# Kernel tuning notes

Hardware: AMD Instinct MI355X
Metric: run time of the kernel (lower is better)

## Reference

```python
import jax, jax.numpy as jnp
import numpy as np

N = 500000      # active voxels
C_IN = 16       # input voxel feature dim
# encoder channels per stage: 32, 64, 128


def setup_inputs() -> dict:
    key = jax.random.key(0)
    ks = jax.random.split(key, 16)

    def w(k, i, o):
        return jax.random.normal(k, (i, o), dtype=jnp.float32) * (1.0 / np.sqrt(i))

    d = {}
    d['feat'] = jax.random.normal(ks[0], (N, C_IN), dtype=jnp.float32)
    d['coords'] = jax.random.randint(ks[1], (N, 4), 0, 1024, dtype=jnp.int32)
    d['W_in'] = w(ks[2], C_IN, 32)
    d['W_enc1'] = w(ks[3], 32, 32)
    d['W_enc2'] = w(ks[4], 32, 64)
    d['W_enc3'] = w(ks[5], 64, 128)
    d['W_lat1'] = w(ks[6], 32, 32)
    d['W_lat2'] = w(ks[7], 64, 64)
    d['W_lat3'] = w(ks[8], 128, 128)
    d['W_merge1'] = w(ks[9], 64, 32)    # merge: 2*C_i -> C_i
    d['W_merge2'] = w(ks[10], 128, 64)
    d['W_merge3'] = w(ks[11], 256, 128)
    d['W_up1'] = w(ks[12], 32, 32)      # upsample: C_i -> C_{i-1}
    d['W_up2'] = w(ks[13], 64, 32)
    d['W_up3'] = w(ks[14], 128, 64)
    return d


def _forward(feat, W_in, W_enc1, W_enc2, W_enc3, W_lat1, W_lat2, W_lat3,
             W_merge1, W_merge2, W_merge3, W_up1, W_up2, W_up3):
    relu = jax.nn.relu
    # conv_input + encoder (1x1 submanifold sparse convs == per-voxel matmul)
    x = relu(feat @ W_in)
    e1 = relu(x @ W_enc1)
    e2 = relu(e1 @ W_enc2)
    e3 = relu(e2 @ W_enc3)
    enc = [e1, e2, e3]
    lats = [W_lat1, W_lat2, W_lat3]
    mrgs = [W_merge1, W_merge2, W_merge3]
    ups = [W_up1, W_up2, W_up3]
    x = e3
    for i in (2, 1, 0):  # decoder stages stage_num..1
        lat = relu(enc[i] @ lats[i])                    # lateral_layer
        # cat0(x_bottom) + cat1(lat): identity-placement 1x1 convs == concat
        cat = jnp.concatenate([x, lat], axis=-1)        # [N, 2*C_i]
        merge = relu(cat @ mrgs[i])                     # merge_layer 2C->C
        red = cat.reshape(cat.shape[0], -1, 2).sum(-1)  # reduce_channel: fixed pairwise-sum conv
        x = relu((merge + red) @ ups[i])                # residual add + upsample_layer
    return x  # ret['voxel_feats']


def reference(feat, coords, W_in, W_enc1, W_enc2, W_enc3, W_lat1, W_lat2, W_lat3,
              W_merge1, W_merge2, W_merge3, W_up1, W_up2, W_up3):
    # coords define sparse structure; for 1x1 subm convs the math only touches features
    return _forward(feat, W_in, W_enc1, W_enc2, W_enc3, W_lat1, W_lat2, W_lat3,
                    W_merge1, W_merge2, W_merge3, W_up1, W_up2, W_up3)
```

## Files before the change

kernel.cpp:

```cpp
#include <hip/hip_runtime.h>

typedef unsigned short u16;
typedef unsigned int u32;
typedef _Float16 h16;
typedef __attribute__((ext_vector_type(2))) _Float16 half2v;
typedef __attribute__((ext_vector_type(8))) _Float16 half8;
typedef __attribute__((ext_vector_type(8))) unsigned short ushort8;
typedef __attribute__((ext_vector_type(4))) float f32x4;

#define NPAIRS 15625
#define STRIPH 12032

#define AE1 0
#define SE1 40
#define AE2 1280
#define SE2 72
#define ACT 3584
#define SCT 264
#define AMR 3712
#define SMR 264

#define MFMA16(A,B,C) __builtin_amdgcn_mfma_f32_16x16x32_f16(A,B,C,0,0,0)

#define LBAR() asm volatile("s_waitcnt lgkmcnt(0)\n\ts_barrier" ::: "memory")

#define F_L0   0
#define F_L1   2
#define F_L2   4
#define F_L3   8
#define F_L4   24
#define F_L5   56
#define F_L6   120
#define F_L7   136
#define F_L8   144
#define F_L9   160
#define F_L10  164
#define F_L11  166
#define F_L12  170
#define NFRAG  172

__device__ __forceinline__ u16 hb(h16 h) { union { h16 h; u16 u; } v; v.h = h; return v.u; }

__global__ __launch_bounds__(256) void pack_w(
    const float* w0, const float* w1, const float* w2, const float* w3, const float* w4,
    const float* w5, const float* w6, const float* w7, const float* w8, const float* w9,
    const float* w10, const float* w11, const float* w12, u16* __restrict__ packed)
{
  const float* ws[13] = {w0,w1,w2,w3,w4,w5,w6,w7,w8,w9,w10,w11,w12};
  const int Ka[13]  = {16,32,32,64,128,256,128,64,128,64,32,64,32};
  const int KT[13]  = {1,1,1,2,4,8,4,2,4,2,1,2,1};
  const int CO[13]  = {32,32,64,128,128,128,64,64,64,32,32,32,32};
  const int FO[13]  = {F_L0,F_L1,F_L2,F_L3,F_L4,F_L5,F_L6,F_L7,F_L8,F_L9,F_L10,F_L11,F_L12};
  int g = blockIdx.x * 256 + threadIdx.x;
  int f = g >> 6, lane = g & 63;
  if (f >= NFRAG) return;
  int layer = 0;
#pragma unroll
  for (int i = 1; i < 13; ++i) if (f >= FO[i]) layer = i;
  int fl = f - FO[layer];
  int kt = fl % KT[layer];
  int ct = fl / KT[layer];
  int cout = CO[layer];
  int quad = lane >> 4;
  int col  = ct * 16 + (lane & 15);
  u16 thi[8], tlo[8];
#pragma unroll
  for (int j = 0; j < 8; ++j) {
    int k = kt * 32 + quad * 8 + j;
    float w = (k < Ka[layer]) ? ws[layer][k * cout + col] : 0.f;
    h16 h = (h16)w;
    h16 l = (h16)(w - (float)h);
    thi[j] = hb(h); tlo[j] = hb(l);
  }
  u16* dst = packed + ((size_t)f * 64 + lane) * 16;
  *(ushort8*)dst       = *(const ushort8*)thi;
  *(ushort8*)(dst + 8) = *(const ushort8*)tlo;
}


__device__ __forceinline__ void splitw(h16* dst, int idx, int dlo, float v) {
  h16 h = (h16)v;
  dst[idx]       = h;
  dst[idx + dlo] = (h16)(v - (float)h);
}

__device__ __forceinline__ float red2p(const h16* cat, int cs, int rr, int cc) {
  half2v hp = *reinterpret_cast<const half2v*>(cat + rr * cs + 2 * cc);
  half2v lp = *reinterpret_cast<const half2v*>(cat + (rr + 16) * cs + 2 * cc);
  return (float)hp.x + (float)hp.y + (float)lp.x + (float)lp.y;
}

template<int KT, int EPI, int BAR>
__device__ __forceinline__ void layerW(
    const h16* __restrict__ asrc, int as,
    const h16* __restrict__ wp, int foff, int ct, int lane,
    half8 pbh, half8 pbl,
    h16* dst, int ds, int colb, const h16* cat, int cs,
    float* __restrict__ gout, int row0)
{
  const int l15 = lane & 15, quad = lane >> 4;
  const int abase = l15 * as + quad * 8;
  const int alo = 16 * as;
  f32x4 a0 = {0.f,0.f,0.f,0.f}, a1 = {0.f,0.f,0.f,0.f};
#pragma unroll
  for (int kt = 0; kt < KT; ++kt) {
    half8 bhv, blv;
    if (kt == 0) { bhv = pbh; blv = pbl; }
    else {
      const h16* fp = wp + (((size_t)(foff + ct * KT + kt)) * 64 + lane) * 16;
      bhv = *(const half8*)fp;
      blv = *(const half8*)(fp + 8);
    }
    const h16* p0 = asrc + abase + kt * 32;
    const h16* p1 = p0 + STRIPH;
    half8 ah0 = *(const half8*)p0;
    half8 al0 = *(const half8*)(p0 + alo);
    half8 ah1 = *(const half8*)p1;
    half8 al1 = *(const half8*)(p1 + alo);
    a0 = MFMA16(al0, bhv, a0); a0 = MFMA16(ah0, blv, a0); a0 = MFMA16(ah0, bhv, a0);
    a1 = MFMA16(al1, bhv, a1); a1 = MFMA16(ah1, blv, a1); a1 = MFMA16(ah1, bhv, a1);
  }
  const int cc = ct * 16 + l15;
  float v0r[4], v1r[4];
#pragma unroll
  for (int r = 0; r < 4; ++r) {
    const int rr = quad * 4 + r;
    float v0 = a0[r] > 0.f ? a0[r] : 0.f;
    float v1 = a1[r] > 0.f ? a1[r] : 0.f;
    if (EPI == 1) {
      v0 += red2p(cat, cs, rr, cc);
      v1 += red2p(cat + STRIPH, cs, rr, cc);
    }
    v0r[r] = v0; v1r[r] = v1;
  }
  if (BAR) LBAR();
  if (EPI <= 1) {
    const int dlo = 16 * ds;
#pragma unroll
    for (int r = 0; r < 4; ++r) {
      const int rr = quad * 4 + r;
      const int idx = rr * ds + colb + cc;
      splitw(dst,          idx, dlo, v0r[r]);
      splitw(dst + STRIPH, idx, dlo, v1r[r]);
    }
  } else {
#pragma unroll
    for (int r = 0; r < 4; ++r) {
      const int rr = quad * 4 + r;
      gout[(size_t)(row0 + rr) * 32 + cc]      = v0r[r];
      gout[(size_t)(row0 + 16 + rr) * 32 + cc] = v1r[r];
    }
  }
}

#define PFB(FOFF, CIDX, KT_)                                                        \
  do { const h16* _fp = wp + (((size_t)((FOFF) + (CIDX) * (KT_))) * 64 + lane) * 16; \
       pbh = *(const half8*)_fp; pbl = *(const half8*)(_fp + 8); } while (0)

__global__ __launch_bounds__(512, 6) void backbone(
    const float* __restrict__ feat, const h16* __restrict__ wp, float* __restrict__ out)
{
  __shared__ h16 lds[2 * STRIPH];
  const int lane = threadIdx.x & 63;
  const int wv   = threadIdx.x >> 6;
  const int l15 = lane & 15, quad = lane >> 4;
  const int row0 = blockIdx.x * 32;

  h16* E1 = lds + AE1;
  h16* E2 = lds + AE2;
  h16* CT = lds + ACT;
  h16* MR = lds + AMR;

  half8 pbh, pbl;

  if (wv < 2) {
    PFB(F_L0, wv, 1);
    h16 th0[8] = {0,0,0,0,0,0,0,0}, tl0[8] = {0,0,0,0,0,0,0,0};
    h16 th1[8] = {0,0,0,0,0,0,0,0}, tl1[8] = {0,0,0,0,0,0,0,0};
    if (quad < 2) {
      const float* s0 = feat + (size_t)(row0 + l15) * 16 + quad * 8;
      const float* s1 = feat + (size_t)(row0 + 16 + l15) * 16 + quad * 8;
      f32x4 u0a = *(const f32x4*)s0, u0b = *(const f32x4*)(s0 + 4);
      f32x4 u1a = *(const f32x4*)s1, u1b = *(const f32x4*)(s1 + 4);
#pragma unroll
      for (int j = 0; j < 4; ++j) {
        h16 h;
        h = (h16)u0a[j]; th0[j]   = h; tl0[j]   = (h16)(u0a[j] - (float)h);
        h = (h16)u0b[j]; th0[4+j] = h; tl0[4+j] = (h16)(u0b[j] - (float)h);
        h = (h16)u1a[j]; th1[j]   = h; tl1[j]   = (h16)(u1a[j] - (float)h);
        h = (h16)u1b[j]; th1[4+j] = h; tl1[4+j] = (h16)(u1b[j] - (float)h);
      }
    }
    half8 ah0 = *(const half8*)th0, al0 = *(const half8*)tl0;
    half8 ah1 = *(const half8*)th1, al1 = *(const half8*)tl1;
    f32x4 a0 = {0.f,0.f,0.f,0.f}, a1 = {0.f,0.f,0.f,0.f};
    a0 = MFMA16(al0, pbh, a0); a0 = MFMA16(ah0, pbl, a0); a0 = MFMA16(ah0, pbh, a0);
    a1 = MFMA16(al1, pbh, a1); a1 = MFMA16(ah1, pbl, a1); a1 = MFMA16(ah1, pbh, a1);
    const int dlo = 16 * SCT;
#pragma unroll
    for (int r = 0; r < 4; ++r) {
      const int rr = quad * 4 + r;
      const int idx = rr * SCT + wv * 16 + l15;
      splitw(CT,          idx, dlo, a0[r] > 0.f ? a0[r] : 0.f);
      splitw(CT + STRIPH, idx, dlo, a1[r] > 0.f ? a1[r] : 0.f);
    }
    PFB(F_L1, wv, 1);
  }
  LBAR();

  if (wv < 2) {
    layerW<1,0,0>(CT,SCT, wp, F_L1, wv, lane, pbh,pbl, E1,SE1,0, nullptr,0, nullptr,0);
  }
  if (wv < 4) PFB(F_L2, wv, 1);
  LBAR();

  if (wv < 4) {
    layerW<1,0,0>(E1,SE1, wp, F_L2, wv, lane, pbh,pbl, E2,SE2,0, nullptr,0, nullptr,0);
  }
  PFB(F_L3, wv, 2);
  LBAR();

  layerW<2,0,0>(E2,SE2, wp, F_L3, wv, lane, pbh,pbl, CT,SCT,0, nullptr,0, nullptr,0);
  PFB(F_L4, wv, 4);
  LBAR();

  layerW<4,0,0>(CT,SCT, wp, F_L4, wv, lane, pbh,pbl, CT,SCT,128, nullptr,0, nullptr,0);
  PFB(F_L5, wv, 8);
  LBAR();

  layerW<8,1,1>(CT,SCT, wp, F_L5, wv, lane, pbh,pbl, MR,SMR,0, CT,SCT, nullptr,0);
  if (wv < 4) PFB(F_L6, wv, 4); else PFB(F_L7, wv - 4, 2);
  LBAR();

  if (wv < 4) {
    layerW<4,0,0>(MR,SMR, wp, F_L6, wv, lane, pbh,pbl, CT,SCT,0,  nullptr,0, nullptr,0);
  } else {
    layerW<2,0,0>(E2,SE2, wp, F_L7, wv - 4, lane, pbh,pbl, CT,SCT,64, nullptr,0, nullptr,0);
  }
  if (wv < 4) PFB(F_L8, wv, 4);
  LBAR();

  if (wv < 4) {
    layerW<4,1,0>(CT,SCT, wp, F_L8, wv, lane, pbh,pbl, MR,SMR,0, CT,SCT, nullptr,0);
  }
  if (wv < 2) PFB(F_L9, wv, 2);
  else if (wv < 4) PFB(F_L10, wv - 2, 1);
  LBAR();

  if (wv < 2) {
    layerW<2,0,0>(MR,SMR, wp, F_L9, wv, lane, pbh,pbl, CT,SCT,0,  nullptr,0, nullptr,0);
  } else if (wv < 4) {
    layerW<1,0,0>(E1,SE1, wp, F_L10, wv - 2, lane, pbh,pbl, CT,SCT,32, nullptr,0, nullptr,0);
  }
  if (wv < 2) PFB(F_L11, wv, 2);
  LBAR();

  if (wv < 2) {
    layerW<2,1,0>(CT,SCT, wp, F_L11, wv, lane, pbh,pbl, MR,SMR,0, CT,SCT, nullptr,0);
    PFB(F_L12, wv, 1);
  }
  LBAR();

  if (wv < 2) {
    layerW<1,2,0>(MR,SMR, wp, F_L12, wv, lane, pbh,pbl, nullptr,0,0, nullptr,0, out, row0);
  }
}

extern "C" void kernel_launch(void* const* d_in, const int* in_sizes, int n_in,
                              void* d_out, int out_size, void* d_ws, size_t ws_size,
                              hipStream_t stream) {
  (void)in_sizes; (void)n_in; (void)out_size; (void)ws_size;
  u16* packed = (u16*)d_ws;

  hipLaunchKernelGGL(pack_w, dim3(43), dim3(256), 0, stream,
      (const float*)d_in[2],  (const float*)d_in[3],  (const float*)d_in[4],
      (const float*)d_in[5],  (const float*)d_in[8],  (const float*)d_in[11],
      (const float*)d_in[14], (const float*)d_in[7],  (const float*)d_in[10],
      (const float*)d_in[13], (const float*)d_in[6],  (const float*)d_in[9],
      (const float*)d_in[12], packed);

  hipLaunchKernelGGL(backbone, dim3(NPAIRS), dim3(512), 0, stream,
                     (const float*)d_in[0], (const h16*)packed, (float*)d_out);
}
```

Before: 432.3 us.

## Remap warp work so each wave computes two column tiles for one row strip

Each wave used to compute one 16-column output tile for both 16-row strips, sharing one B fragment across two A fragments. Now each wave handles one row strip and two adjacent column tiles, so one A fragment (hi/lo) is reused across two weight fragments. This doubles the weight loads per wave and halves the LDS activation reads. It also spreads the first layer over four waves instead of two. The change shifts the bottleneck from LDS reads toward global/L2 weight fetches and adds more prefetch registers.

Result: slower. 459.8 us (+6.4%).

```diff
diff --git a/kernel.cpp b/kernel.cpp
--- a/kernel.cpp
+++ b/kernel.cpp
@@ -91,45 +91,43 @@
 }
 
 template<int KT, int EPI, int BAR>
-__device__ __forceinline__ void layerW(
+__device__ __forceinline__ void layer1(
     const h16* __restrict__ asrc, int as,
-    const h16* __restrict__ wp, int foff, int ct, int lane,
-    half8 pbh, half8 pbl,
+    const h16* __restrict__ wp, int foff, int ct0, int lane,
+    half8 pbh, half8 pbl, half8 pbh2, half8 pbl2,
     h16* dst, int ds, int colb, const h16* cat, int cs,
-    float* __restrict__ gout, int row0)
+    float* __restrict__ gout, int grow0)
 {
   const int l15 = lane & 15, quad = lane >> 4;
   const int abase = l15 * as + quad * 8;
   const int alo = 16 * as;
-  f32x4 a0 = {0.f,0.f,0.f,0.f}, a1 = {0.f,0.f,0.f,0.f};
+  f32x4 acc0 = {0.f,0.f,0.f,0.f}, acc1 = {0.f,0.f,0.f,0.f};
 #pragma unroll
   for (int kt = 0; kt < KT; ++kt) {
-    half8 bhv, blv;
-    if (kt == 0) { bhv = pbh; blv = pbl; }
+    const h16* p0 = asrc + abase + kt * 32;
+    half8 ah = *(const half8*)p0;
+    half8 al = *(const half8*)(p0 + alo);
+    half8 b0h, b0l, b1h, b1l;
+    if (kt == 0) { b0h = pbh; b0l = pbl; b1h = pbh2; b1l = pbl2; }
     else {
-      const h16* fp = wp + (((size_t)(foff + ct * KT + kt)) * 64 + lane) * 16;
-      bhv = *(const half8*)fp;
-      blv = *(const half8*)(fp + 8);
-    }
-    const h16* p0 = asrc + abase + kt * 32;
-    const h16* p1 = p0 + STRIPH;
-    half8 ah0 = *(const half8*)p0;
-    half8 al0 = *(const half8*)(p0 + alo);
-    half8 ah1 = *(const half8*)p1;
-    half8 al1 = *(const half8*)(p1 + alo);
-    a0 = MFMA16(al0, bhv, a0); a0 = MFMA16(ah0, blv, a0); a0 = MFMA16(ah0, bhv, a0);
-    a1 = MFMA16(al1, bhv, a1); a1 = MFMA16(ah1, blv, a1); a1 = MFMA16(ah1, bhv, a1);
-  }
-  const int cc = ct * 16 + l15;
+      const h16* f0 = wp + (((size_t)(foff + ct0 * KT + kt)) * 64 + lane) * 16;
+      const h16* f1 = wp + (((size_t)(foff + (ct0 + 1) * KT + kt)) * 64 + lane) * 16;
+      b0h = *(const half8*)f0; b0l = *(const half8*)(f0 + 8);
+      b1h = *(const half8*)f1; b1l = *(const half8*)(f1 + 8);
+    }
+    acc0 = MFMA16(al, b0h, acc0); acc0 = MFMA16(ah, b0l, acc0); acc0 = MFMA16(ah, b0h, acc0);
+    acc1 = MFMA16(al, b1h, acc1); acc1 = MFMA16(ah, b1l, acc1); acc1 = MFMA16(ah, b1h, acc1);
+  }
+  const int cc0 = ct0 * 16 + l15, cc1 = cc0 + 16;
   float v0r[4], v1r[4];
 #pragma unroll
   for (int r = 0; r < 4; ++r) {
     const int rr = quad * 4 + r;
-    float v0 = a0[r] > 0.f ? a0[r] : 0.f;
-    float v1 = a1[r] > 0.f ? a1[r] : 0.f;
+    float v0 = acc0[r] > 0.f ? acc0[r] : 0.f;
+    float v1 = acc1[r] > 0.f ? acc1[r] : 0.f;
     if (EPI == 1) {
-      v0 += red2p(cat, cs, rr, cc);
-      v1 += red2p(cat + STRIPH, cs, rr, cc);
+      v0 += red2p(cat, cs, rr, cc0);
+      v1 += red2p(cat, cs, rr, cc1);
     }
     v0r[r] = v0; v1r[r] = v1;
   }
@@ -139,16 +137,15 @@
 #pragma unroll
     for (int r = 0; r < 4; ++r) {
       const int rr = quad * 4 + r;
-      const int idx = rr * ds + colb + cc;
-      splitw(dst,          idx, dlo, v0r[r]);
-      splitw(dst + STRIPH, idx, dlo, v1r[r]);
+      splitw(dst, rr * ds + colb + cc0, dlo, v0r[r]);
+      splitw(dst, rr * ds + colb + cc1, dlo, v1r[r]);
     }
   } else {
 #pragma unroll
     for (int r = 0; r < 4; ++r) {
       const int rr = quad * 4 + r;
-      gout[(size_t)(row0 + rr) * 32 + cc]      = v0r[r];
-      gout[(size_t)(row0 + 16 + rr) * 32 + cc] = v1r[r];
+      gout[(size_t)(grow0 + rr) * 32 + cc0] = v0r[r];
+      gout[(size_t)(grow0 + rr) * 32 + cc1] = v1r[r];
     }
   }
 }
@@ -156,6 +153,9 @@
 #define PFB(FOFF, CIDX, KT_)                                                        \
   do { const h16* _fp = wp + (((size_t)((FOFF) + (CIDX) * (KT_))) * 64 + lane) * 16; \
        pbh = *(const half8*)_fp; pbl = *(const half8*)(_fp + 8); } while (0)
+#define PFB2(FOFF, CIDX, KT_)                                                       \
+  do { const h16* _fp = wp + (((size_t)((FOFF) + (CIDX) * (KT_))) * 64 + lane) * 16; \
+       pbh2 = *(const half8*)_fp; pbl2 = *(const half8*)(_fp + 8); } while (0)
 
 __global__ __launch_bounds__(512, 6) void backbone(
     const float* __restrict__ feat, const h16* __restrict__ wp, float* __restrict__ out)
@@ -165,104 +165,114 @@
   const int wv   = threadIdx.x >> 6;
   const int l15 = lane & 15, quad = lane >> 4;
   const int row0 = blockIdx.x * 32;
-
-  h16* E1 = lds + AE1;
-  h16* E2 = lds + AE2;
-  h16* CT = lds + ACT;
-  h16* MR = lds + AMR;
-
-  half8 pbh, pbl;
-
-  if (wv < 2) {
-    PFB(F_L0, wv, 1);
-    h16 th0[8] = {0,0,0,0,0,0,0,0}, tl0[8] = {0,0,0,0,0,0,0,0};
-    h16 th1[8] = {0,0,0,0,0,0,0,0}, tl1[8] = {0,0,0,0,0,0,0,0};
+  const int c2 = (wv >> 1) * 2;
+  h16* Sb8 = lds + (wv & 1) * STRIPH;
+
+  half8 pbh, pbl, pbh2, pbl2;
+
+  if (wv < 4) {
+    const int st = wv >> 1, ct = wv & 1;
+    PFB(F_L0, ct, 1);
+    h16 th[8] = {0,0,0,0,0,0,0,0}, tl[8] = {0,0,0,0,0,0,0,0};
     if (quad < 2) {
-      const float* s0 = feat + (size_t)(row0 + l15) * 16 + quad * 8;
-      const float* s1 = feat + (size_t)(row0 + 16 + l15) * 16 + quad * 8;
-      f32x4 u0a = *(const f32x4*)s0, u0b = *(const f32x4*)(s0 + 4);
-      f32x4 u1a = *(const f32x4*)s1, u1b = *(const f32x4*)(s1 + 4);
+      const float* s = feat + (size_t)(row0 + st * 16 + l15) * 16 + quad * 8;
+      f32x4 ua = *(const f32x4*)s, ub = *(const f32x4*)(s + 4);
 #pragma unroll
       for (int j = 0; j < 4; ++j) {
         h16 h;
-        h = (h16)u0a[j]; th0[j]   = h; tl0[j]   = (h16)(u0a[j] - (float)h);
-        h = (h16)u0b[j]; th0[4+j] = h; tl0[4+j] = (h16)(u0b[j] - (float)h);
-        h = (h16)u1a[j]; th1[j]   = h; tl1[j]   = (h16)(u1a[j] - (float)h);
-        h = (h16)u1b[j]; th1[4+j] = h; tl1[4+j] = (h16)(u1b[j] - (float)h);
+        h = (h16)ua[j]; th[j]   = h; tl[j]   = (h16)(ua[j] - (float)h);
+        h = (h16)ub[j]; th[4+j] = h; tl[4+j] = (h16)(ub[j] - (float)h);
       }
     }
-    half8 ah0 = *(const half8*)th0, al0 = *(const half8*)tl0;
-    half8 ah1 = *(const half8*)th1, al1 = *(const half8*)tl1;
-    f32x4 a0 = {0.f,0.f,0.f,0.f}, a1 = {0.f,0.f,0.f,0.f};
-    a0 = MFMA16(al0, pbh, a0); a0 = MFMA16(ah0, pbl, a0); a0 = MFMA16(ah0, pbh, a0);
-    a1 = MFMA16(al1, pbh, a1); a1 = MFMA16(ah1, pbl, a1); a1 = MFMA16(ah1, pbh, a1);
+    half8 ah = *(const half8*)th, al = *(const half8*)tl;
+    f32x4 a = {0.f,0.f,0.f,0.f};
+    a = MFMA16(al, pbh, a); a = MFMA16(ah, pbl, a); a = MFMA16(ah, pbh, a);
+    h16* dstS = lds + st * STRIPH + ACT;
     const int dlo = 16 * SCT;
 #pragma unroll
     for (int r = 0; r < 4; ++r) {
       const int rr = quad * 4 + r;
-      const int idx = rr * SCT + wv * 16 + l15;
-      splitw(CT,          idx, dlo, a0[r] > 0.f ? a0[r] : 0.f);
-      splitw(CT + STRIPH, idx, dlo, a1[r] > 0.f ? a1[r] : 0.f);
-    }
-    PFB(F_L1, wv, 1);
-  }
-  LBAR();
-
-  if (wv < 2) {
-    layerW<1,0,0>(CT,SCT, wp, F_L1, wv, lane, pbh,pbl, E1,SE1,0, nullptr,0, nullptr,0);
-  }
-  if (wv < 4) PFB(F_L2, wv, 1);
-  LBAR();
-
-  if (wv < 4) {
-    layerW<1,0,0>(E1,SE1, wp, F_L2, wv, lane, pbh,pbl, E2,SE2,0, nullptr,0, nullptr,0);
-  }
-  PFB(F_L3, wv, 2);
-  LBAR();
-
-  layerW<2,0,0>(E2,SE2, wp, F_L3, wv, lane, pbh,pbl, CT,SCT,0, nullptr,0, nullptr,0);
-  PFB(F_L4, wv, 4);
-  LBAR();
-
-  layerW<4,0,0>(CT,SCT, wp, F_L4, wv, lane, pbh,pbl, CT,SCT,128, nullptr,0, nullptr,0);
-  PFB(F_L5, wv, 8);
-  LBAR();
-
-  layerW<8,1,1>(CT,SCT, wp, F_L5, wv, lane, pbh,pbl, MR,SMR,0, CT,SCT, nullptr,0);
-  if (wv < 4) PFB(F_L6, wv, 4); else PFB(F_L7, wv - 4, 2);
-  LBAR();
-
-  if (wv < 4) {
-    layerW<4,0,0>(MR,SMR, wp, F_L6, wv, lane, pbh,pbl, CT,SCT,0,  nullptr,0, nullptr,0);
+      splitw(dstS, rr * SCT + ct * 16 + l15, dlo, a[r] > 0.f ? a[r] : 0.f);
+    }
+  }
+  if (wv < 2) { PFB(F_L1, 0, 1); PFB2(F_L1, 1, 1); }
+  LBAR();
+
+  if (wv < 2) {
+    h16* Sb = lds + wv * STRIPH;
+    layer1<1,0,0>(Sb + ACT, SCT, wp, F_L1, 0, lane, pbh,pbl,pbh2,pbl2,
+                  Sb + AE1, SE1, 0, nullptr, 0, nullptr, 0);
+  }
+  if (wv < 4) { PFB(F_L2, c2, 1); PFB2(F_L2, c2 + 1, 1); }
+  LBAR();
+
+  if (wv < 4) {
+    layer1<1,0,0>(Sb8 + AE1, SE1, wp, F_L2, c2, lane, pbh,pbl,pbh2,pbl2,
+                  Sb8 + AE2, SE2, 0, nullptr, 0, nullptr, 0);
+  }
+  PFB(F_L3, c2, 2); PFB2(F_L3, c2 + 1, 2);
+  LBAR();
+
+  layer1<2,0,0>(Sb8 + AE2, SE2, wp, F_L3, c2, lane, pbh,pbl,pbh2,pbl2,
+                Sb8 + ACT, SCT, 0, nullptr, 0, nullptr, 0);
+  PFB(F_L4, c2, 4); PFB2(F_L4, c2 + 1, 4);
+  LBAR();
+
+  layer1<4,0,0>(Sb8 + ACT, SCT, wp, F_L4, c2, lane, pbh,pbl,pbh2,pbl2,
+                Sb8 + ACT, SCT, 128, nullptr, 0, nullptr, 0);
+  PFB(F_L5, c2, 8); PFB2(F_L5, c2 + 1, 8);
+  LBAR();
+
+  layer1<8,1,1>(Sb8 + ACT, SCT, wp, F_L5, c2, lane, pbh,pbl,pbh2,pbl2,
+                Sb8 + AMR, SMR, 0, Sb8 + ACT, SCT, nullptr, 0);
+  if (wv < 4) { PFB(F_L6, c2, 4); PFB2(F_L6, c2 + 1, 4); }
+  else        { const int w = wv - 4; PFB(F_L7, (w>>1)*2, 2); PFB2(F_L7, (w>>1)*2 + 1, 2); }
+  LBAR();
+
+  if (wv < 4) {
+    layer1<4,0,0>(Sb8 + AMR, SMR, wp, F_L6, c2, lane, pbh,pbl,pbh2,pbl2,
+                  Sb8 + ACT, SCT, 0, nullptr, 0, nullptr, 0);
   } else {
-    layerW<2,0,0>(E2,SE2, wp, F_L7, wv - 4, lane, pbh,pbl, CT,SCT,64, nullptr,0, nullptr,0);
-  }
-  if (wv < 4) PFB(F_L8, wv, 4);
-  LBAR();
-
-  if (wv < 4) {
-    layerW<4,1,0>(CT,SCT, wp, F_L8, wv, lane, pbh,pbl, MR,SMR,0, CT,SCT, nullptr,0);
-  }
-  if (wv < 2) PFB(F_L9, wv, 2);
-  else if (wv < 4) PFB(F_L10, wv - 2, 1);
-  LBAR();
-
-  if (wv < 2) {
-    layerW<2,0,0>(MR,SMR, wp, F_L9, wv, lane, pbh,pbl, CT,SCT,0,  nullptr,0, nullptr,0);
+    const int w = wv - 4;
+    h16* Sb = lds + (w & 1) * STRIPH;
+    layer1<2,0,0>(Sb + AE2, SE2, wp, F_L7, (w>>1)*2, lane, pbh,pbl,pbh2,pbl2,
+                  Sb + ACT, SCT, 64, nullptr, 0, nullptr, 0);
+  }
+  if (wv < 4) { PFB(F_L8, c2, 4); PFB2(F_L8, c2 + 1, 4); }
+  LBAR();
+
+  if (wv < 4) {
+    layer1<4,1,0>(Sb8 + ACT, SCT, wp, F_L8, c2, lane, pbh,pbl,pbh2,pbl2,
+                  Sb8 + AMR, SMR, 0, Sb8 + ACT, SCT, nullptr, 0);
+  }
+  if (wv < 2)      { PFB(F_L9, 0, 2);  PFB2(F_L9, 1, 2); }
+  else if (wv < 4) { PFB(F_L10, 0, 1); PFB2(F_L10, 1, 1); }
+  LBAR();
+
+  if (wv < 2) {
+    h16* Sb = lds + wv * STRIPH;
+    layer1<2,0,0>(Sb + AMR, SMR, wp, F_L9, 0, lane, pbh,pbl,pbh2,pbl2,
+                  Sb + ACT, SCT, 0, nullptr, 0, nullptr, 0);
   } else if (wv < 4) {
-    layerW<1,0,0>(E1,SE1, wp, F_L10, wv - 2, lane, pbh,pbl, CT,SCT,32, nullptr,0, nullptr,0);
-  }
-  if (wv < 2) PFB(F_L11, wv, 2);
-  LBAR();
-
-  if (wv < 2) {
-    layerW<2,1,0>(CT,SCT, wp, F_L11, wv, lane, pbh,pbl, MR,SMR,0, CT,SCT, nullptr,0);
-    PFB(F_L12, wv, 1);
-  }
-  LBAR();
-
-  if (wv < 2) {
-    layerW<1,2,0>(MR,SMR, wp, F_L12, wv, lane, pbh,pbl, nullptr,0,0, nullptr,0, out, row0);
+    h16* Sb = lds + (wv - 2) * STRIPH;
+    layer1<1,0,0>(Sb + AE1, SE1, wp, F_L10, 0, lane, pbh,pbl,pbh2,pbl2,
+                  Sb + ACT, SCT, 32, nullptr, 0, nullptr, 0);
+  }
+  if (wv < 2) { PFB(F_L11, 0, 2); PFB2(F_L11, 1, 2); }
+  LBAR();
+
+  if (wv < 2) {
+    h16* Sb = lds + wv * STRIPH;
+    layer1<2,1,0>(Sb + ACT, SCT, wp, F_L11, 0, lane, pbh,pbl,pbh2,pbl2,
+                  Sb + AMR, SMR, 0, Sb + ACT, SCT, nullptr, 0);
+    PFB(F_L12, 0, 1); PFB2(F_L12, 1, 1);
+  }
+  LBAR();
+
+  if (wv < 2) {
+    h16* Sb = lds + wv * STRIPH;
+    layer1<1,2,0>(Sb + AMR, SMR, wp, F_L12, 0, lane, pbh,pbl,pbh2,pbl2,
+                  nullptr, 0, 0, nullptr, 0, out, row0 + wv * 16);
   }
 }
 
```

## Split narrow layers across strips per wave and swizzle LDS columns

Applied to the files above, without the earlier changes.

Narrow layers used to run on only 2 or 4 waves, each handling both 16-row strips. They now run on twice as many waves, each handling a single strip (unitS), so more waves do useful work at those stages. The lat2/merge2 stage is fused so all 8 waves run both pieces back to back, using a second prefetched weight register pair. An XOR swizzle is also applied to the LDS column indices on both read and write, aimed at reducing bank conflicts. The cost is more register pressure from the extra prefetch and more complicated indexing that must stay consistent for correctness.

Measured after the change: 438.3 us. Within noise of the previous version (+1.4%).

```diff
diff --git a/kernel.cpp b/kernel.cpp
--- a/kernel.cpp
+++ b/kernel.cpp
@@ -84,9 +84,9 @@
   dst[idx + dlo] = (h16)(v - (float)h);
 }
 
-__device__ __forceinline__ float red2p(const h16* cat, int cs, int rr, int cc) {
-  half2v hp = *reinterpret_cast<const half2v*>(cat + rr * cs + 2 * cc);
-  half2v lp = *reinterpret_cast<const half2v*>(cat + (rr + 16) * cs + 2 * cc);
+__device__ __forceinline__ float red2s(const h16* cat, int cs, int rr, int ccr) {
+  half2v hp = *reinterpret_cast<const half2v*>(cat + rr * cs + ccr);
+  half2v lp = *reinterpret_cast<const half2v*>(cat + (rr + 16) * cs + ccr);
   return (float)hp.x + (float)hp.y + (float)lp.x + (float)lp.y;
 }
 
@@ -99,7 +99,8 @@
     float* __restrict__ gout, int row0)
 {
   const int l15 = lane & 15, quad = lane >> 4;
-  const int abase = l15 * as + quad * 8;
+  const int qsw = quad ^ ((l15 >> 3) << 1);
+  const int abase = l15 * as + qsw * 8;
   const int alo = 16 * as;
   f32x4 a0 = {0.f,0.f,0.f,0.f}, a1 = {0.f,0.f,0.f,0.f};
 #pragma unroll
@@ -120,7 +121,10 @@
     a0 = MFMA16(al0, bhv, a0); a0 = MFMA16(ah0, blv, a0); a0 = MFMA16(ah0, bhv, a0);
     a1 = MFMA16(al1, bhv, a1); a1 = MFMA16(ah1, blv, a1); a1 = MFMA16(ah1, bhv, a1);
   }
-  const int cc = ct * 16 + l15;
+  const int csw = (quad & 2) << 3;
+  const int cc  = ct * 16 + l15;
+  const int ccw = (colb + cc) ^ csw;
+  const int ccr = (2 * cc) ^ csw;
   float v0r[4], v1r[4];
 #pragma unroll
   for (int r = 0; r < 4; ++r) {
@@ -128,8 +132,8 @@
     float v0 = a0[r] > 0.f ? a0[r] : 0.f;
     float v1 = a1[r] > 0.f ? a1[r] : 0.f;
     if (EPI == 1) {
-      v0 += red2p(cat, cs, rr, cc);
-      v1 += red2p(cat + STRIPH, cs, rr, cc);
+      v0 += red2s(cat, cs, rr, ccr);
+      v1 += red2s(cat + STRIPH, cs, rr, ccr);
     }
     v0r[r] = v0; v1r[r] = v1;
   }
@@ -139,9 +143,8 @@
 #pragma unroll
     for (int r = 0; r < 4; ++r) {
       const int rr = quad * 4 + r;
-      const int idx = rr * ds + colb + cc;
-      splitw(dst,          idx, dlo, v0r[r]);
-      splitw(dst + STRIPH, idx, dlo, v1r[r]);
+      splitw(dst,          rr * ds + ccw, dlo, v0r[r]);
+      splitw(dst + STRIPH, rr * ds + ccw, dlo, v1r[r]);
     }
   } else {
 #pragma unroll
@@ -149,6 +152,62 @@
       const int rr = quad * 4 + r;
       gout[(size_t)(row0 + rr) * 32 + cc]      = v0r[r];
       gout[(size_t)(row0 + 16 + rr) * 32 + cc] = v1r[r];
+    }
+  }
+}
+
+template<int KT, int EPI, int BAR>
+__device__ __forceinline__ void unitS(
+    const h16* __restrict__ asrc, int as,
+    const h16* __restrict__ wp, int foff, int ct, int lane,
+    half8 pbh, half8 pbl,
+    h16* dst, int ds, int colb, const h16* cat, int cs,
+    float* __restrict__ gout, int grow0)
+{
+  const int l15 = lane & 15, quad = lane >> 4;
+  const int qsw = quad ^ ((l15 >> 3) << 1);
+  const int abase = l15 * as + qsw * 8;
+  const int alo = 16 * as;
+  f32x4 a = {0.f,0.f,0.f,0.f};
+#pragma unroll
+  for (int kt = 0; kt < KT; ++kt) {
+    half8 bhv, blv;
+    if (kt == 0) { bhv = pbh; blv = pbl; }
+    else {
+      const h16* fp = wp + (((size_t)(foff + ct * KT + kt)) * 64 + lane) * 16;
+      bhv = *(const half8*)fp;
+      blv = *(const half8*)(fp + 8);
+    }
+    const h16* p0 = asrc + abase + kt * 32;
+    half8 ah = *(const half8*)p0;
+    half8 al = *(const half8*)(p0 + alo);
+    a = MFMA16(al, bhv, a); a = MFMA16(ah, blv, a); a = MFMA16(ah, bhv, a);
+  }
+  const int csw = (quad & 2) << 3;
+  const int cc  = ct * 16 + l15;
+  const int ccw = (colb + cc) ^ csw;
+  const int ccr = (2 * cc) ^ csw;
+  float vr[4];
+#pragma unroll
+  for (int r = 0; r < 4; ++r) {
+    const int rr = quad * 4 + r;
+    float v = a[r] > 0.f ? a[r] : 0.f;
+    if (EPI == 1) v += red2s(cat, cs, rr, ccr);
+    vr[r] = v;
+  }
+  if (BAR) LBAR();
+  if (EPI <= 1) {
+    const int dlo = 16 * ds;
+#pragma unroll
+    for (int r = 0; r < 4; ++r) {
+      const int rr = quad * 4 + r;
+      splitw(dst, rr * ds + ccw, dlo, vr[r]);
+    }
+  } else {
+#pragma unroll
+    for (int r = 0; r < 4; ++r) {
+      const int rr = quad * 4 + r;
+      gout[(size_t)(grow0 + rr) * 32 + cc] = vr[r];
     }
   }
 }
@@ -156,6 +215,9 @@
 #define PFB(FOFF, CIDX, KT_)                                                        \
   do { const h16* _fp = wp + (((size_t)((FOFF) + (CIDX) * (KT_))) * 64 + lane) * 16; \
        pbh = *(const half8*)_fp; pbl = *(const half8*)(_fp + 8); } while (0)
+#define PFB2(FOFF, CIDX, KT_)                                                       \
+  do { const h16* _fp = wp + (((size_t)((FOFF) + (CIDX) * (KT_))) * 64 + lane) * 16; \
+       pbh2 = *(const half8*)_fp; pbl2 = *(const half8*)(_fp + 8); } while (0)
 
 __global__ __launch_bounds__(512, 6) void backbone(
     const float* __restrict__ feat, const h16* __restrict__ wp, float* __restrict__ out)
@@ -171,98 +233,117 @@
   h16* CT = lds + ACT;
   h16* MR = lds + AMR;
 
-  half8 pbh, pbl;
-
-  if (wv < 2) {
-    PFB(F_L0, wv, 1);
-    h16 th0[8] = {0,0,0,0,0,0,0,0}, tl0[8] = {0,0,0,0,0,0,0,0};
-    h16 th1[8] = {0,0,0,0,0,0,0,0}, tl1[8] = {0,0,0,0,0,0,0,0};
+  half8 pbh, pbl, pbh2, pbl2;
+
+  if (wv < 4) {
+    const int s = wv >> 1, c = wv & 1;
+    PFB(F_L0, c, 1);
+    h16 th[8] = {0,0,0,0,0,0,0,0}, tl[8] = {0,0,0,0,0,0,0,0};
     if (quad < 2) {
-      const float* s0 = feat + (size_t)(row0 + l15) * 16 + quad * 8;
-      const float* s1 = feat + (size_t)(row0 + 16 + l15) * 16 + quad * 8;
-      f32x4 u0a = *(const f32x4*)s0, u0b = *(const f32x4*)(s0 + 4);
-      f32x4 u1a = *(const f32x4*)s1, u1b = *(const f32x4*)(s1 + 4);
+      const float* sp = feat + (size_t)(row0 + s * 16 + l15) * 16 + quad * 8;
+      f32x4 ua = *(const f32x4*)sp, ub = *(const f32x4*)(sp + 4);
 #pragma unroll
       for (int j = 0; j < 4; ++j) {
         h16 h;
-        h = (h16)u0a[j]; th0[j]   = h; tl0[j]   = (h16)(u0a[j] - (float)h);
-        h = (h16)u0b[j]; th0[4+j] = h; tl0[4+j] = (h16)(u0b[j] - (float)h);
-        h = (h16)u1a[j]; th1[j]   = h; tl1[j]   = (h16)(u1a[j] - (float)h);
-        h = (h16)u1b[j]; th1[4+j] = h; tl1[4+j] = (h16)(u1b[j] - (float)h);
+        h = (h16)ua[j]; th[j]   = h; tl[j]   = (h16)(ua[j] - (float)h);
+        h = (h16)ub[j]; th[4+j] = h; tl[4+j] = (h16)(ub[j] - (float)h);
       }
     }
-    half8 ah0 = *(const half8*)th0, al0 = *(const half8*)tl0;
-    half8 ah1 = *(const half8*)th1, al1 = *(const half8*)tl1;
-    f32x4 a0 = {0.f,0.f,0.f,0.f}, a1 = {0.f,0.f,0.f,0.f};
-    a0 = MFMA16(al0, pbh, a0); a0 = MFMA16(ah0, pbl, a0); a0 = MFMA16(ah0, pbh, a0);
-    a1 = MFMA16(al1, pbh, a1); a1 = MFMA16(ah1, pbl, a1); a1 = MFMA16(ah1, pbh, a1);
+    half8 ah = *(const half8*)th, al = *(const half8*)tl;
+    f32x4 a = {0.f,0.f,0.f,0.f};
+    a = MFMA16(al, pbh, a); a = MFMA16(ah, pbl, a); a = MFMA16(ah, pbh, a);
+    h16* dstS = lds + s * STRIPH + ACT;
+    const int csw = (quad & 2) << 3;
+    const int ccw = (c * 16 + l15) ^ csw;
     const int dlo = 16 * SCT;
 #pragma unroll
     for (int r = 0; r < 4; ++r) {
       const int rr = quad * 4 + r;
-      const int idx = rr * SCT + wv * 16 + l15;
-      splitw(CT,          idx, dlo, a0[r] > 0.f ? a0[r] : 0.f);
-      splitw(CT + STRIPH, idx, dlo, a1[r] > 0.f ? a1[r] : 0.f);
-    }
-    PFB(F_L1, wv, 1);
-  }
-  LBAR();
-
-  if (wv < 2) {
-    layerW<1,0,0>(CT,SCT, wp, F_L1, wv, lane, pbh,pbl, E1,SE1,0, nullptr,0, nullptr,0);
-  }
-  if (wv < 4) PFB(F_L2, wv, 1);
-  LBAR();
-
-  if (wv < 4) {
-    layerW<1,0,0>(E1,SE1, wp, F_L2, wv, lane, pbh,pbl, E2,SE2,0, nullptr,0, nullptr,0);
+      splitw(dstS, rr * SCT + ccw, dlo, a[r] > 0.f ? a[r] : 0.f);
+    }
+    PFB(F_L1, c, 1);
+  }
+  LBAR();
+
+  if (wv < 4) {
+    const int s = wv >> 1, c = wv & 1;
+    h16* Sb = lds + s * STRIPH;
+    unitS<1,0,0>(Sb + ACT, SCT, wp, F_L1, c, lane, pbh, pbl,
+                 Sb + AE1, SE1, 0, nullptr, 0, nullptr, 0);
+  }
+  PFB(F_L2, wv & 3, 1);
+  LBAR();
+
+  {
+    const int s = wv >> 2, c = wv & 3;
+    h16* Sb = lds + s * STRIPH;
+    unitS<1,0,0>(Sb + AE1, SE1, wp, F_L2, c, lane, pbh, pbl,
+                 Sb + AE2, SE2, 0, nullptr, 0, nullptr, 0);
   }
   PFB(F_L3, wv, 2);
   LBAR();
 
-  layerW<2,0,0>(E2,SE2, wp, F_L3, wv, lane, pbh,pbl, CT,SCT,0, nullptr,0, nullptr,0);
+  layerW<2,0,0>(E2, SE2, wp, F_L3, wv, lane, pbh, pbl, CT, SCT, 0, nullptr, 0, nullptr, 0);
   PFB(F_L4, wv, 4);
   LBAR();
 
-  layerW<4,0,0>(CT,SCT, wp, F_L4, wv, lane, pbh,pbl, CT,SCT,128, nullptr,0, nullptr,0);
+  layerW<4,0,0>(CT, SCT, wp, F_L4, wv, lane, pbh, pbl, CT, SCT, 128, nullptr, 0, nullptr, 0);
   PFB(F_L5, wv, 8);
   LBAR();
 
-  layerW<8,1,1>(CT,SCT, wp, F_L5, wv, lane, pbh,pbl, MR,SMR,0, CT,SCT, nullptr,0);
-  if (wv < 4) PFB(F_L6, wv, 4); else PFB(F_L7, wv - 4, 2);
-  LBAR();
-
-  if (wv < 4) {
-    layerW<4,0,0>(MR,SMR, wp, F_L6, wv, lane, pbh,pbl, CT,SCT,0,  nullptr,0, nullptr,0);
+  layerW<8,1,1>(CT, SCT, wp, F_L5, wv, lane, pbh, pbl, MR, SMR, 0, CT, SCT, nullptr, 0);
+  PFB (F_L6, wv & 3, 4);
+  PFB2(F_L7, wv & 3, 2);
+  LBAR();
+
+  {
+    const int s = wv >> 2, c = wv & 3;
+    h16* Sb = lds + s * STRIPH;
+    unitS<4,0,0>(Sb + AMR, SMR, wp, F_L6, c, lane, pbh,  pbl,
+                 Sb + ACT, SCT, 0,  nullptr, 0, nullptr, 0);
+    unitS<2,0,0>(Sb + AE2, SE2, wp, F_L7, c, lane, pbh2, pbl2,
+                 Sb + ACT, SCT, 64, nullptr, 0, nullptr, 0);
+  }
+  PFB(F_L8, wv & 3, 4);
+  LBAR();
+
+  {
+    const int s = wv >> 2, c = wv & 3;
+    h16* Sb = lds + s * STRIPH;
+    unitS<4,1,0>(Sb + ACT, SCT, wp, F_L8, c, lane, pbh, pbl,
+                 Sb + AMR, SMR, 0, Sb + ACT, SCT, nullptr, 0);
+  }
+  if (wv < 4) PFB(F_L9, wv & 1, 2); else PFB(F_L10, (wv - 4) & 1, 1);
+  LBAR();
+
+  if (wv < 4) {
+    const int s = wv >> 1, c = wv & 1;
+    h16* Sb = lds + s * STRIPH;
+    unitS<2,0,0>(Sb + AMR, SMR, wp, F_L9, c, lane, pbh, pbl,
+                 Sb + ACT, SCT, 0, nullptr, 0, nullptr, 0);
   } else {
-    layerW<2,0,0>(E2,SE2, wp, F_L7, wv - 4, lane, pbh,pbl, CT,SCT,64, nullptr,0, nullptr,0);
-  }
-  if (wv < 4) PFB(F_L8, wv, 4);
-  LBAR();
-
-  if (wv < 4) {
-    layerW<4,1,0>(CT,SCT, wp, F_L8, wv, lane, pbh,pbl, MR,SMR,0, CT,SCT, nullptr,0);
-  }
-  if (wv < 2) PFB(F_L9, wv, 2);
-  else if (wv < 4) PFB(F_L10, wv - 2, 1);
-  LBAR();
-
-  if (wv < 2) {
-    layerW<2,0,0>(MR,SMR, wp, F_L9, wv, lane, pbh,pbl, CT,SCT,0,  nullptr,0, nullptr,0);
-  } else if (wv < 4) {
-    layerW<1,0,0>(E1,SE1, wp, F_L10, wv - 2, lane, pbh,pbl, CT,SCT,32, nullptr,0, nullptr,0);
-  }
-  if (wv < 2) PFB(F_L11, wv, 2);
-  LBAR();
-
-  if (wv < 2) {
-    layerW<2,1,0>(CT,SCT, wp, F_L11, wv, lane, pbh,pbl, MR,SMR,0, CT,SCT, nullptr,0);
-    PFB(F_L12, wv, 1);
-  }
-  LBAR();
-
-  if (wv < 2) {
-    layerW<1,2,0>(MR,SMR, wp, F_L12, wv, lane, pbh,pbl, nullptr,0,0, nullptr,0, out, row0);
+    const int w = wv - 4, s = w >> 1, c = w & 1;
+    h16* Sb = lds + s * STRIPH;
+    unitS<1,0,0>(Sb + AE1, SE1, wp, F_L10, c, lane, pbh, pbl,
+                 Sb + ACT, SCT, 32, nullptr, 0, nullptr, 0);
+  }
+  if (wv < 4) PFB(F_L11, wv & 1, 2);
+  LBAR();
+
+  if (wv < 4) {
+    const int s = wv >> 1, c = wv & 1;
+    h16* Sb = lds + s * STRIPH;
+    unitS<2,1,0>(Sb + ACT, SCT, wp, F_L11, c, lane, pbh, pbl,
+                 Sb + AMR, SMR, 0, Sb + ACT, SCT, nullptr, 0);
+    PFB(F_L12, c, 1);
+  }
+  LBAR();
+
+  if (wv < 4) {
+    const int s = wv >> 1, c = wv & 1;
+    h16* Sb = lds + s * STRIPH;
+    unitS<1,2,0>(Sb + AMR, SMR, wp, F_L12, c, lane, pbh, pbl,
+                 nullptr, 0, 0, nullptr, 0, out, row0 + s * 16);
   }
 }
 
```

## Switch to 32x32x16 MFMA tiles with 4-wave blocks and fewer barriers

Applied to the files above, without the earlier changes.

Replaces the 16x16x32 MFMA tiling with 32x32x16 MFMA instructions. Each wave now covers all 32 rows of a block per 32-column output tile, so the block shrinks from 8 waves to 4. The weight packing is reorganised to match the new fragment layout. Early and late layers that need only one wave run back to back with a local LDS wait instead of a block barrier, which removes some sync points. In exchange, each wave holds more accumulator state and carries a longer dependent chain, and occupancy hints change.

New measurement: 456.0 us. 1.05x slower.

```diff
diff --git a/kernel.cpp b/kernel.cpp
--- a/kernel.cpp
+++ b/kernel.cpp
@@ -7,6 +7,7 @@
 typedef __attribute__((ext_vector_type(8))) _Float16 half8;
 typedef __attribute__((ext_vector_type(8))) unsigned short ushort8;
 typedef __attribute__((ext_vector_type(4))) float f32x4;
+typedef __attribute__((ext_vector_type(16))) float f32x16;
 
 #define NPAIRS 15625
 #define STRIPH 12032
@@ -20,24 +21,25 @@
 #define AMR 3712
 #define SMR 264
 
-#define MFMA16(A,B,C) __builtin_amdgcn_mfma_f32_16x16x32_f16(A,B,C,0,0,0)
+#define MFMA32(A,B,C) __builtin_amdgcn_mfma_f32_32x32x16_f16(A,B,C,0,0,0)
 
 #define LBAR() asm volatile("s_waitcnt lgkmcnt(0)\n\ts_barrier" ::: "memory")
+#define LWAIT() asm volatile("s_waitcnt lgkmcnt(0)" ::: "memory")
 
 #define F_L0   0
-#define F_L1   2
-#define F_L2   4
-#define F_L3   8
-#define F_L4   24
-#define F_L5   56
-#define F_L6   120
-#define F_L7   136
-#define F_L8   144
-#define F_L9   160
-#define F_L10  164
-#define F_L11  166
-#define F_L12  170
-#define NFRAG  172
+#define F_L1   1
+#define F_L2   3
+#define F_L3   7
+#define F_L4   23
+#define F_L5   55
+#define F_L6   119
+#define F_L7   135
+#define F_L8   143
+#define F_L9   159
+#define F_L10  163
+#define F_L11  165
+#define F_L12  169
+#define NFRAG  171
 
 __device__ __forceinline__ u16 hb(h16 h) { union { h16 h; u16 u; } v; v.h = h; return v.u; }
 
@@ -48,7 +50,7 @@
 {
   const float* ws[13] = {w0,w1,w2,w3,w4,w5,w6,w7,w8,w9,w10,w11,w12};
   const int Ka[13]  = {16,32,32,64,128,256,128,64,128,64,32,64,32};
-  const int KT[13]  = {1,1,1,2,4,8,4,2,4,2,1,2,1};
+  const int KS[13]  = {1,2,2,4,8,16,8,4,8,4,2,4,2};
   const int CO[13]  = {32,32,64,128,128,128,64,64,64,32,32,32,32};
   const int FO[13]  = {F_L0,F_L1,F_L2,F_L3,F_L4,F_L5,F_L6,F_L7,F_L8,F_L9,F_L10,F_L11,F_L12};
   int g = blockIdx.x * 256 + threadIdx.x;
@@ -58,15 +60,14 @@
 #pragma unroll
   for (int i = 1; i < 13; ++i) if (f >= FO[i]) layer = i;
   int fl = f - FO[layer];
-  int kt = fl % KT[layer];
-  int ct = fl / KT[layer];
+  int ks = fl % KS[layer];
+  int ct = fl / KS[layer];
   int cout = CO[layer];
-  int quad = lane >> 4;
-  int col  = ct * 16 + (lane & 15);
+  int col  = ct * 32 + (lane & 31);
   u16 thi[8], tlo[8];
 #pragma unroll
   for (int j = 0; j < 8; ++j) {
-    int k = kt * 32 + quad * 8 + j;
+    int k = ks * 16 + (lane >> 5) * 8 + j;
     float w = (k < Ka[layer]) ? ws[layer][k * cout + col] : 0.f;
     h16 h = (h16)w;
     h16 l = (h16)(w - (float)h);
@@ -84,86 +85,78 @@
   dst[idx + dlo] = (h16)(v - (float)h);
 }
 
-__device__ __forceinline__ float red2p(const h16* cat, int cs, int rr, int cc) {
-  half2v hp = *reinterpret_cast<const half2v*>(cat + rr * cs + 2 * cc);
-  half2v lp = *reinterpret_cast<const half2v*>(cat + (rr + 16) * cs + 2 * cc);
+__device__ __forceinline__ float red2p(const h16* catS, int cs, int r16, int cc) {
+  half2v hp = *reinterpret_cast<const half2v*>(catS + r16 * cs + 2 * cc);
+  half2v lp = *reinterpret_cast<const half2v*>(catS + (r16 + 16) * cs + 2 * cc);
   return (float)hp.x + (float)hp.y + (float)lp.x + (float)lp.y;
 }
 
-template<int KT, int EPI, int BAR>
-__device__ __forceinline__ void layerW(
+template<int KS_, int EPI, int BAR>
+__device__ __forceinline__ void layer32(
     const h16* __restrict__ asrc, int as,
     const h16* __restrict__ wp, int foff, int ct, int lane,
     half8 pbh, half8 pbl,
     h16* dst, int ds, int colb, const h16* cat, int cs,
     float* __restrict__ gout, int row0)
 {
-  const int l15 = lane & 15, quad = lane >> 4;
-  const int abase = l15 * as + quad * 8;
+  const int ra = lane & 31;
+  const int abase = (ra >> 4) * STRIPH + (ra & 15) * as + ((lane >> 5) << 3);
   const int alo = 16 * as;
-  f32x4 a0 = {0.f,0.f,0.f,0.f}, a1 = {0.f,0.f,0.f,0.f};
-#pragma unroll
-  for (int kt = 0; kt < KT; ++kt) {
+  f32x16 acc = {0.f,0.f,0.f,0.f,0.f,0.f,0.f,0.f,0.f,0.f,0.f,0.f,0.f,0.f,0.f,0.f};
+#pragma unroll
+  for (int ks = 0; ks < KS_; ++ks) {
     half8 bhv, blv;
-    if (kt == 0) { bhv = pbh; blv = pbl; }
+    if (ks == 0) { bhv = pbh; blv = pbl; }
     else {
-      const h16* fp = wp + (((size_t)(foff + ct * KT + kt)) * 64 + lane) * 16;
+      const h16* fp = wp + (((size_t)(foff + ct * KS_ + ks)) * 64 + lane) * 16;
       bhv = *(const half8*)fp;
       blv = *(const half8*)(fp + 8);
     }
-    const h16* p0 = asrc + abase + kt * 32;
-    const h16* p1 = p0 + STRIPH;
-    half8 ah0 = *(const half8*)p0;
-    half8 al0 = *(const half8*)(p0 + alo);
-    half8 ah1 = *(const half8*)p1;
-    half8 al1 = *(const half8*)(p1 + alo);
-    a0 = MFMA16(al0, bhv, a0); a0 = MFMA16(ah0, blv, a0); a0 = MFMA16(ah0, bhv, a0);
-    a1 = MFMA16(al1, bhv, a1); a1 = MFMA16(ah1, blv, a1); a1 = MFMA16(ah1, bhv, a1);
-  }
-  const int cc = ct * 16 + l15;
-  float v0r[4], v1r[4];
-#pragma unroll
-  for (int r = 0; r < 4; ++r) {
-    const int rr = quad * 4 + r;
-    float v0 = a0[r] > 0.f ? a0[r] : 0.f;
-    float v1 = a1[r] > 0.f ? a1[r] : 0.f;
-    if (EPI == 1) {
-      v0 += red2p(cat, cs, rr, cc);
-      v1 += red2p(cat + STRIPH, cs, rr, cc);
-    }
-    v0r[r] = v0; v1r[r] = v1;
+    const h16* p = asrc + abase + ks * 16;
+    half8 ah = *(const half8*)p;
+    half8 al = *(const half8*)(p + alo);
+    acc = MFMA32(al, bhv, acc);
+    acc = MFMA32(ah, blv, acc);
+    acc = MFMA32(ah, bhv, acc);
+  }
+  const int cc  = ct * 32 + (lane & 31);
+  const int hl4 = (lane >> 5) << 2;
+  float vr[16];
+#pragma unroll
+  for (int i = 0; i < 16; ++i) {
+    const int rr = (i & 3) + ((i >> 2) << 3) + hl4;
+    float v = acc[i] > 0.f ? acc[i] : 0.f;
+    if (EPI == 1)
+      v += red2p(cat + (rr >> 4) * STRIPH, cs, rr & 15, cc);
+    vr[i] = v;
   }
   if (BAR) LBAR();
   if (EPI <= 1) {
     const int dlo = 16 * ds;
 #pragma unroll
-    for (int r = 0; r < 4; ++r) {
-      const int rr = quad * 4 + r;
-      const int idx = rr * ds + colb + cc;
-      splitw(dst,          idx, dlo, v0r[r]);
-      splitw(dst + STRIPH, idx, dlo, v1r[r]);
+    for (int i = 0; i < 16; ++i) {
+      const int rr = (i & 3) + ((i >> 2) << 3) + hl4;
+      splitw(dst + (rr >> 4) * STRIPH, (rr & 15) * ds + colb + cc, dlo, vr[i]);
     }
   } else {
 #pragma unroll
-    for (int r = 0; r < 4; ++r) {
-      const int rr = quad * 4 + r;
-      gout[(size_t)(row0 + rr) * 32 + cc]      = v0r[r];
-      gout[(size_t)(row0 + 16 + rr) * 32 + cc] = v1r[r];
-    }
-  }
-}
-
-#define PFB(FOFF, CIDX, KT_)                                                        \
-  do { const h16* _fp = wp + (((size_t)((FOFF) + (CIDX) * (KT_))) * 64 + lane) * 16; \
+    for (int i = 0; i < 16; ++i) {
+      const int rr = (i & 3) + ((i >> 2) << 3) + hl4;
+      gout[(size_t)(row0 + rr) * 32 + cc] = vr[i];
+    }
+  }
+}
+
+#define PFB(FOFF, CIDX, KS_)                                                        \
+  do { const h16* _fp = wp + (((size_t)((FOFF) + (CIDX) * (KS_))) * 64 + lane) * 16; \
        pbh = *(const half8*)_fp; pbl = *(const half8*)(_fp + 8); } while (0)
 
-__global__ __launch_bounds__(512, 6) void backbone(
+__global__ __launch_bounds__(256, 3) void backbone(
     const float* __restrict__ feat, const h16* __restrict__ wp, float* __restrict__ out)
 {
   __shared__ h16 lds[2 * STRIPH];
   const int lane = threadIdx.x & 63;
   const int wv   = threadIdx.x >> 6;
-  const int l15 = lane & 15, quad = lane >> 4;
   const int row0 = blockIdx.x * 32;
 
   h16* E1 = lds + AE1;
@@ -173,96 +166,83 @@
 
   half8 pbh, pbl;
 
+  if (wv == 0) {
+    PFB(F_L0, 0, 1);
+    const int ra = lane & 31;
+    const float* sp = feat + (size_t)(row0 + ra) * 16 + ((lane >> 5) << 3);
+    f32x4 ua = *(const f32x4*)sp, ub = *(const f32x4*)(sp + 4);
+    h16 th[8], tl[8];
+#pragma unroll
+    for (int j = 0; j < 4; ++j) {
+      h16 h;
+      h = (h16)ua[j]; th[j]   = h; tl[j]   = (h16)(ua[j] - (float)h);
+      h = (h16)ub[j]; th[4+j] = h; tl[4+j] = (h16)(ub[j] - (float)h);
+    }
+    half8 ah = *(const half8*)th, al = *(const half8*)tl;
+    f32x16 a = {0.f,0.f,0.f,0.f,0.f,0.f,0.f,0.f,0.f,0.f,0.f,0.f,0.f,0.f,0.f,0.f};
+    a = MFMA32(al, pbh, a); a = MFMA32(ah, pbl, a); a = MFMA32(ah, pbh, a);
+    const int cl = lane & 31, hl4 = (lane >> 5) << 2;
+    const int dlo = 16 * SCT;
+#pragma unroll
+    for (int i = 0; i < 16; ++i) {
+      const int rr = (i & 3) + ((i >> 2) << 3) + hl4;
+      splitw(CT + (rr >> 4) * STRIPH, (rr & 15) * SCT + cl, dlo, a[i] > 0.f ? a[i] : 0.f);
+    }
+    PFB(F_L1, 0, 2);
+    LWAIT();
+    layer32<2,0,0>(CT, SCT, wp, F_L1, 0, lane, pbh, pbl, E1, SE1, 0, nullptr, 0, nullptr, 0);
+    PFB(F_L2, 0, 2);
+  } else if (wv == 1) {
+    PFB(F_L2, 1, 2);
+  }
+  LBAR();
+
   if (wv < 2) {
-    PFB(F_L0, wv, 1);
-    h16 th0[8] = {0,0,0,0,0,0,0,0}, tl0[8] = {0,0,0,0,0,0,0,0};
-    h16 th1[8] = {0,0,0,0,0,0,0,0}, tl1[8] = {0,0,0,0,0,0,0,0};
-    if (quad < 2) {
-      const float* s0 = feat + (size_t)(row0 + l15) * 16 + quad * 8;
-      const float* s1 = feat + (size_t)(row0 + 16 + l15) * 16 + quad * 8;
-      f32x4 u0a = *(const f32x4*)s0, u0b = *(const f32x4*)(s0 + 4);
-      f32x4 u1a = *(const f32x4*)s1, u1b = *(const f32x4*)(s1 + 4);
-#pragma unroll
-      for (int j = 0; j < 4; ++j) {
-        h16 h;
-        h = (h16)u0a[j]; th0[j]   = h; tl0[j]   = (h16)(u0a[j] - (float)h);
-        h = (h16)u0b[j]; th0[4+j] = h; tl0[4+j] = (h16)(u0b[j] - (float)h);
-        h = (h16)u1a[j]; th1[j]   = h; tl1[j]   = (h16)(u1a[j] - (float)h);
-        h = (h16)u1b[j]; th1[4+j] = h; tl1[4+j] = (h16)(u1b[j] - (float)h);
-      }
-    }
-    half8 ah0 = *(const half8*)th0, al0 = *(const half8*)tl0;
-    half8 ah1 = *(const half8*)th1, al1 = *(const half8*)tl1;
-    f32x4 a0 = {0.f,0.f,0.f,0.f}, a1 = {0.f,0.f,0.f,0.f};
-    a0 = MFMA16(al0, pbh, a0); a0 = MFMA16(ah0, pbl, a0); a0 = MFMA16(ah0, pbh, a0);
-    a1 = MFMA16(al1, pbh, a1); a1 = MFMA16(ah1, pbl, a1); a1 = MFMA16(ah1, pbh, a1);
-    const int dlo = 16 * SCT;
-#pragma unroll
-    for (int r = 0; r < 4; ++r) {
-      const int rr = quad * 4 + r;
-      const int idx = rr * SCT + wv * 16 + l15;
-      splitw(CT,          idx, dlo, a0[r] > 0.f ? a0[r] : 0.f);
-      splitw(CT + STRIPH, idx, dlo, a1[r] > 0.f ? a1[r] : 0.f);
-    }
-    PFB(F_L1, wv, 1);
-  }
+    layer32<2,0,0>(E1, SE1, wp, F_L2, wv, lane, pbh, pbl, E2, SE2, 0, nullptr, 0, nullptr, 0);
+  }
+  PFB(F_L3, wv, 4);
+  LBAR();
+
+  layer32<4,0,0>(E2, SE2, wp, F_L3, wv, lane, pbh, pbl, CT, SCT, 0, nullptr, 0, nullptr, 0);
+  PFB(F_L4, wv, 8);
+  LBAR();
+
+  layer32<8,0,0>(CT, SCT, wp, F_L4, wv, lane, pbh, pbl, CT, SCT, 128, nullptr, 0, nullptr, 0);
+  PFB(F_L5, wv, 16);
+  LBAR();
+
+  layer32<16,1,1>(CT, SCT, wp, F_L5, wv, lane, pbh, pbl, MR, SMR, 0, CT, SCT, nullptr, 0);
+  if (wv < 2) PFB(F_L6, wv, 8); else PFB(F_L7, wv - 2, 4);
   LBAR();
 
   if (wv < 2) {
-    layerW<1,0,0>(CT,SCT, wp, F_L1, wv, lane, pbh,pbl, E1,SE1,0, nullptr,0, nullptr,0);
-  }
-  if (wv < 4) PFB(F_L2, wv, 1);
-  LBAR();
-
-  if (wv < 4) {
-    layerW<1,0,0>(E1,SE1, wp, F_L2, wv, lane, pbh,pbl, E2,SE2,0, nullptr,0, nullptr,0);
-  }
-  PFB(F_L3, wv, 2);
-  LBAR();
-
-  layerW<2,0,0>(E2,SE2, wp, F_L3, wv, lane, pbh,pbl, CT,SCT,0, nullptr,0, nullptr,0);
-  PFB(F_L4, wv, 4);
-  LBAR();
-
-  layerW<4,0,0>(CT,SCT, wp, F_L4, wv, lane, pbh,pbl, CT,SCT,128, nullptr,0, nullptr,0);
-  PFB(F_L5, wv, 8);
-  LBAR();
-
-  layerW<8,1,1>(CT,SCT, wp, F_L5, wv, lane, pbh,pbl, MR,SMR,0, CT,SCT, nullptr,0);
-  if (wv < 4) PFB(F_L6, wv, 4); else PFB(F_L7, wv - 4, 2);
-  LBAR();
-
-  if (wv < 4) {
-    layerW<4,0,0>(MR,SMR, wp, F_L6, wv, lane, pbh,pbl, CT,SCT,0,  nullptr,0, nullptr,0);
+    layer32<8,0,0>(MR, SMR, wp, F_L6, wv, lane, pbh, pbl, CT, SCT, 0, nullptr, 0, nullptr, 0);
+    PFB(F_L8, wv, 8);
   } else {
-    layerW<2,0,0>(E2,SE2, wp, F_L7, wv - 4, lane, pbh,pbl, CT,SCT,64, nullptr,0, nullptr,0);
-  }
-  if (wv < 4) PFB(F_L8, wv, 4);
-  LBAR();
-
-  if (wv < 4) {
-    layerW<4,1,0>(CT,SCT, wp, F_L8, wv, lane, pbh,pbl, MR,SMR,0, CT,SCT, nullptr,0);
-  }
-  if (wv < 2) PFB(F_L9, wv, 2);
-  else if (wv < 4) PFB(F_L10, wv - 2, 1);
+    layer32<4,0,0>(E2, SE2, wp, F_L7, wv - 2, lane, pbh, pbl, CT, SCT, 64, nullptr, 0, nullptr, 0);
+  }
   LBAR();
 
   if (wv < 2) {
-    layerW<2,0,0>(MR,SMR, wp, F_L9, wv, lane, pbh,pbl, CT,SCT,0,  nullptr,0, nullptr,0);
-  } else if (wv < 4) {
-    layerW<1,0,0>(E1,SE1, wp, F_L10, wv - 2, lane, pbh,pbl, CT,SCT,32, nullptr,0, nullptr,0);
-  }
-  if (wv < 2) PFB(F_L11, wv, 2);
-  LBAR();
-
-  if (wv < 2) {
-    layerW<2,1,0>(CT,SCT, wp, F_L11, wv, lane, pbh,pbl, MR,SMR,0, CT,SCT, nullptr,0);
-    PFB(F_L12, wv, 1);
-  }
-  LBAR();
-
-  if (wv < 2) {
-    layerW<1,2,0>(MR,SMR, wp, F_L12, wv, lane, pbh,pbl, nullptr,0,0, nullptr,0, out, row0);
+    layer32<8,1,0>(CT, SCT, wp, F_L8, wv, lane, pbh, pbl, MR, SMR, 0, CT, SCT, nullptr, 0);
+  }
+  if (wv == 0) PFB(F_L9, 0, 4);
+  else if (wv == 1) PFB(F_L10, 0, 2);
+  LBAR();
+
+  if (wv == 0) {
+    layer32<4,0,0>(MR, SMR, wp, F_L9, 0, lane, pbh, pbl, CT, SCT, 0, nullptr, 0, nullptr, 0);
+    PFB(F_L11, 0, 4);
+  } else if (wv == 1) {
+    layer32<2,0,0>(E1, SE1, wp, F_L10, 0, lane, pbh, pbl, CT, SCT, 32, nullptr, 0, nullptr, 0);
+  }
+  LBAR();
+
+  if (wv == 0) {
+    layer32<4,1,0>(CT, SCT, wp, F_L11, 0, lane, pbh, pbl, MR, SMR, 0, CT, SCT, nullptr, 0);
+    PFB(F_L12, 0, 2);
+    LWAIT();
+    layer32<2,2,0>(MR, SMR, wp, F_L12, 0, lane, pbh, pbl, nullptr, 0, 0, nullptr, 0, out, row0);
   }
 }
 
@@ -279,6 +259,6 @@
       (const float*)d_in[13], (const float*)d_in[6],  (const float*)d_in[9],
       (const float*)d_in[12], packed);
 
-  hipLaunchKernelGGL(backbone, dim3(NPAIRS), dim3(512), 0, stream,
+  hipLaunchKernelGGL(backbone, dim3(NPAIRS), dim3(256), 0, stream,
                      (const float*)d_in[0], (const h16*)packed, (float*)d_out);
 }
```
